# Performance work log

Measured on AMD Instinct MI355X. Metric: run time of the kernel, lower is better.

Reference implementation:

```python
import jax, jax.numpy as jnp
import numpy as np

D_MODEL = 1024
D_STATE = 16
D_CONV = 4
EXPAND = 2
D_INNER = EXPAND * D_MODEL          # 2048
DT_RANK = (D_MODEL + 15) // 16      # 64 (mamba 'auto')
B, L = 2, 1024


def _mamba_params(key, scale=0.02):
    ks = jax.random.split(key, 6)
    return dict(
        inW=jax.random.normal(ks[0], (2 * D_INNER, D_MODEL), jnp.float32) * scale,
        convW=jax.random.normal(ks[1], (D_INNER, 1, D_CONV), jnp.float32) * scale,
        convb=jnp.zeros((D_INNER,), jnp.float32),
        xprojW=jax.random.normal(ks[2], (DT_RANK + 2 * D_STATE, D_INNER), jnp.float32) * scale,
        dtW=jax.random.normal(ks[3], (D_INNER, DT_RANK), jnp.float32) * scale,
        dtb=jax.random.normal(ks[4], (D_INNER,), jnp.float32) * scale,
        A_log=jnp.log(jnp.tile(jnp.arange(1, D_STATE + 1, dtype=jnp.float32), (D_INNER, 1))),
        Dskip=jnp.ones((D_INNER,), jnp.float32),
        outW=jax.random.normal(ks[5], (D_MODEL, D_INNER), jnp.float32) * scale,
    )


def setup_inputs() -> dict:
    key = jax.random.key(0)
    kx, kf, kb, kp = jax.random.split(key, 4)
    inp = {"x": jax.random.normal(kx, (B, L, D_MODEL), jnp.float32)}
    inp["ln_w"] = jnp.ones((D_MODEL,), jnp.float32)
    inp["ln_b"] = jnp.zeros((D_MODEL,), jnp.float32)
    for pref, k in (("f_", kf), ("b_", kb)):
        for name, v in _mamba_params(k).items():
            inp[pref + name] = v
    inp["proj_W"] = jax.random.normal(kp, (D_MODEL, 2 * D_MODEL), jnp.float32) * 0.02
    inp["proj_b"] = jnp.zeros((D_MODEL,), jnp.float32)
    return inp


def _layernorm(x, w, b, eps=1e-5):
    mu = jnp.mean(x, axis=-1, keepdims=True)
    var = jnp.var(x, axis=-1, keepdims=True)
    return (x - mu) * jax.lax.rsqrt(var + eps) * w + b


def _mamba(x, inW, convW, convb, xprojW, dtW, dtb, A_log, Dskip, outW):
    # x: [B, L, d_model]
    xz = jnp.einsum('bld,ed->ble', x, inW)           # [B,L,2*d_inner]
    xs, z = jnp.split(xz, 2, axis=-1)                # each [B,L,d_inner]
    # depthwise causal conv over L
    xc = jnp.transpose(xs, (0, 2, 1))                # [B,d_inner,L]
    xc = jax.lax.conv_general_dilated(
        xc, convW, window_strides=(1,), padding=[(D_CONV - 1, 0)],
        feature_group_count=D_INNER)
    xs = jax.nn.silu(jnp.transpose(xc + convb[None, :, None], (0, 2, 1)))
    # input-dependent dt, B, C
    xdb = jnp.einsum('bld,ed->ble', xs, xprojW)      # [B,L,dt_rank+2*d_state]
    dt, Bm, Cm = jnp.split(xdb, [DT_RANK, DT_RANK + D_STATE], axis=-1)
    dt = jax.nn.softplus(jnp.einsum('blr,dr->bld', dt, dtW) + dtb)  # [B,L,d_inner]
    A = -jnp.exp(A_log)                              # [d_inner,d_state], negative
    dA = jnp.exp(dt[..., None] * A)                  # [B,L,d_inner,d_state]
    dBx = dt[..., None] * Bm[:, :, None, :] * xs[..., None]

    def step(h, inputs):
        dA_t, dBx_t, C_t = inputs                    # [B,d,s],[B,d,s],[B,s]
        h = h * dA_t + dBx_t
        y = jnp.einsum('bds,bs->bd', h, C_t)
        return h, y

    h0 = jnp.zeros((x.shape[0], D_INNER, D_STATE), x.dtype)
    _, ys = jax.lax.scan(step, h0, (jnp.moveaxis(dA, 1, 0),
                                    jnp.moveaxis(dBx, 1, 0),
                                    jnp.moveaxis(Cm, 1, 0)))
    y = jnp.moveaxis(ys, 0, 1)                       # [B,L,d_inner]
    y = (y + xs * Dskip) * jax.nn.silu(z)
    return jnp.einsum('bld,ed->ble', y, outW)        # [B,L,d_model]


def reference(x, ln_w, ln_b,
              f_inW, f_convW, f_convb, f_xprojW, f_dtW, f_dtb, f_A_log, f_Dskip, f_outW,
              b_inW, b_convW, b_convb, b_xprojW, b_dtW, b_dtb, b_A_log, b_Dskip, b_outW,
              proj_W, proj_b):
    normed = _layernorm(x, ln_w, ln_b)
    fwd_out = _mamba(normed, f_inW, f_convW, f_convb, f_xprojW, f_dtW, f_dtb,
                     f_A_log, f_Dskip, f_outW)
    bwd_out = _mamba(normed[:, ::-1, :], b_inW, b_convW, b_convb, b_xprojW, b_dtW,
                     b_dtb, b_A_log, b_Dskip, b_outW)[:, ::-1, :]
    combined = jnp.concatenate([fwd_out, bwd_out], axis=-1)
    return x + jnp.einsum('blc,ec->ble', combined, proj_W) + proj_b
```

## Files before the change

kernel.cpp:

```cpp
#include <hip/hip_runtime.h>
#include <hip/hip_bf16.h>
#include <math.h>

#define DM   1024
#define DI   2048
#define DTR  64
#define DST  16
#define NB   2
#define LL   1024
#define MR   (NB*LL)
#define XLD  128
#define KS   8

typedef __bf16 bf16x8 __attribute__((ext_vector_type(8)));
typedef float  f32x4  __attribute__((ext_vector_type(4)));

__device__ __forceinline__ float siluf(float x) { return x / (1.f + __expf(-x)); }
__device__ __forceinline__ float softplusf(float x) {
    return fmaxf(x, 0.f) + log1pf(__expf(-fabsf(x)));
}
__device__ __forceinline__ unsigned short f2bf(float f) {
    __hip_bfloat16 h = __float2bfloat16(f);
    return *reinterpret_cast<unsigned short*>(&h);
}
__device__ __forceinline__ float bf2f(__hip_bfloat16 h) { return __bfloat162float(h); }

__device__ __forceinline__ void gl2lds16(const __hip_bfloat16* g, __hip_bfloat16* l)
{
    __builtin_amdgcn_global_load_lds(
        (const __attribute__((address_space(1))) unsigned int*)g,
        (__attribute__((address_space(3))) unsigned int*)l, 16, 0, 0);
}

__global__ __launch_bounds__(256) void layernorm_k(
    const float* __restrict__ x, const float* __restrict__ w,
    const float* __restrict__ b, __hip_bfloat16* __restrict__ out)
{
    int row = blockIdx.x;
    int tid = threadIdx.x;
    const float* xr = x + (size_t)row * DM;
    float4 v = *(const float4*)(xr + tid * 4);
    float s = v.x + v.y + v.z + v.w;
    float q = v.x*v.x + v.y*v.y + v.z*v.z + v.w*v.w;
    #pragma unroll
    for (int off = 32; off > 0; off >>= 1) {
        s += __shfl_xor(s, off, 64);
        q += __shfl_xor(q, off, 64);
    }
    __shared__ float ss[4], qq[4];
    int wv = tid >> 6;
    if ((tid & 63) == 0) { ss[wv] = s; qq[wv] = q; }
    __syncthreads();
    s = ss[0] + ss[1] + ss[2] + ss[3];
    q = qq[0] + qq[1] + qq[2] + qq[3];
    float mu  = s * (1.f / DM);
    float var = q * (1.f / DM) - mu * mu;
    float rstd = rsqrtf(var + 1e-5f);
    float4 wv4 = *(const float4*)(w + tid * 4);
    float4 bv4 = *(const float4*)(b + tid * 4);
    ushort4 o;
    o.x = f2bf((v.x - mu) * rstd * wv4.x + bv4.x);
    o.y = f2bf((v.y - mu) * rstd * wv4.y + bv4.y);
    o.z = f2bf((v.z - mu) * rstd * wv4.z + bv4.z);
    o.w = f2bf((v.w - mu) * rstd * wv4.w + bv4.w);
    *(ushort4*)((unsigned short*)out + (size_t)row * DM + tid * 4) = o;
}

__global__ __launch_bounds__(256) void cvt_all_k(
    const float* __restrict__ s0, const float* __restrict__ s1,
    const float* __restrict__ s2, const float* __restrict__ s3,
    const float* __restrict__ s4, __hip_bfloat16* __restrict__ dst)
{
    long idx = (long)(blockIdx.x * 256 + threadIdx.x) * 4;
    const float* src; long off;
    if      (idx <  4194304L) { src = s0; off = idx; }
    else if (idx <  8388608L) { src = s1; off = idx -  4194304L; }
    else if (idx < 10485760L) { src = s2; off = idx -  8388608L; }
    else if (idx < 12582912L) { src = s3; off = idx - 10485760L; }
    else                      { src = s4; off = idx - 12582912L; }
    float4 v = *(const float4*)(src + off);
    ushort4 o;
    o.x = f2bf(v.x); o.y = f2bf(v.y); o.z = f2bf(v.z); o.w = f2bf(v.w);
    *(ushort4*)((unsigned short*)dst + idx) = o;
}

__global__ __launch_bounds__(256) void cvt_pad96_k(
    const float* __restrict__ f_in, const float* __restrict__ b_in,
    __hip_bfloat16* __restrict__ out)
{
    int z = blockIdx.y;
    const float* in = z ? b_in : f_in;
    int idx = (blockIdx.x * 256 + threadIdx.x) * 4;
    int row = idx >> 11;
    ushort4 o = make_ushort4(0, 0, 0, 0);
    if (row < 96) {
        float4 v = *(const float4*)(in + idx);
        o.x = f2bf(v.x); o.y = f2bf(v.y); o.z = f2bf(v.z); o.w = f2bf(v.w);
    }
    *(ushort4*)((unsigned short*)out + (size_t)z * 128 * DI + idx) = o;
}

template<int EPI>
__global__ __launch_bounds__(256) void gemm_gl(
    const __hip_bfloat16* __restrict__ A, int lda, size_t astride,
    const __hip_bfloat16* __restrict__ B, int ldb, size_t bstride,
    void* __restrict__ Cp, int ldc, size_t cstride, int K,
    const float* __restrict__ bias,
    const float* __restrict__ res, int ldres)
{
    __shared__ __hip_bfloat16 As[128 * 64];
    __shared__ __hip_bfloat16 Bs[128 * 64];
    const int tid  = threadIdx.x;
    const int z    = blockIdx.z;
    const int bm   = blockIdx.y * 128;
    const int bn   = blockIdx.x * 128;
    const __hip_bfloat16* Az = A + (size_t)z * astride;
    const __hip_bfloat16* Bz = B + (size_t)z * bstride;
    const int wv   = tid >> 6;
    const int lane = tid & 63;
    const int wr   = (wv >> 1) * 64;
    const int wc   = (wv & 1) * 64;
    const int srow = wv * 32 + (lane >> 3);
    const int cg   = ((lane & 7) ^ (lane >> 3)) * 8;
    const int fr   = lane & 15;
    const int quad = lane >> 4;
    const int pc0  = (quad ^ (fr & 7)) * 8;
    const int pc1  = ((4 + quad) ^ (fr & 7)) * 8;

    f32x4 acc[4][4] = {};

    for (int k0 = 0; k0 < K; k0 += 64) {
        __syncthreads();
        #pragma unroll
        for (int i = 0; i < 4; ++i) {
            int r = srow + i * 8;
            gl2lds16(Az + (size_t)(bm + r) * lda + k0 + cg, As + wv * 2048 + i * 512);
            gl2lds16(Bz + (size_t)(bn + r) * ldb + k0 + cg, Bs + wv * 2048 + i * 512);
        }
        __syncthreads();
        #pragma unroll
        for (int kk = 0; kk < 2; ++kk) {
            const int pc = kk ? pc1 : pc0;
            bf16x8 af[4], bf_[4];
            #pragma unroll
            for (int i = 0; i < 4; ++i) {
                af[i]  = *(const bf16x8*)(As + (wr + i * 16 + fr) * 64 + pc);
                bf_[i] = *(const bf16x8*)(Bs + (wc + i * 16 + fr) * 64 + pc);
            }
            #pragma unroll
            for (int i = 0; i < 4; ++i)
                #pragma unroll
                for (int j = 0; j < 4; ++j)
                    acc[i][j] = __builtin_amdgcn_mfma_f32_16x16x32_bf16(
                        af[i], bf_[j], acc[i][j], 0, 0, 0);
        }
    }

    const int er = quad * 4;
    const int ec = fr;
    #pragma unroll
    for (int i = 0; i < 4; ++i) {
        #pragma unroll
        for (int j = 0; j < 4; ++j) {
            int row = bm + wr + i * 16 + er;
            int col = bn + wc + j * 16 + ec;
            #pragma unroll
            for (int r = 0; r < 4; ++r) {
                float v = acc[i][j][r];
                if (EPI == 1) {
                    ((__hip_bfloat16*)Cp)[(size_t)z * cstride +
                        (size_t)(row + r) * ldc + col] = __float2bfloat16(v);
                } else {
                    ((float*)Cp)[(size_t)(row + r) * ldc + col] =
                        v + bias[col] + res[(size_t)(row + r) * ldres + col];
                }
            }
        }
    }
}

__global__ __launch_bounds__(256) void xproj_part_k(
    const __hip_bfloat16* __restrict__ A,
    const __hip_bfloat16* __restrict__ B,
    float* __restrict__ part)
{
    __shared__ __hip_bfloat16 As[128 * 64];
    __shared__ __hip_bfloat16 Bs[128 * 64];
    const int tid  = threadIdx.x;
    const int ks   = blockIdx.x;
    const int bm   = blockIdx.y * 128;
    const int z    = blockIdx.z;
    const __hip_bfloat16* Az = A + (size_t)z * MR * DI;
    const __hip_bfloat16* Bz = B + (size_t)z * 128 * DI;
    const int kb   = ks * (DI / KS);
    const int wv   = tid >> 6;
    const int lane = tid & 63;
    const int wr   = (wv >> 1) * 64;
    const int wc   = (wv & 1) * 64;
    const int srow = wv * 32 + (lane >> 3);
    const int cg   = ((lane & 7) ^ (lane >> 3)) * 8;
    const int fr   = lane & 15;
    const int quad = lane >> 4;
    const int pc0  = (quad ^ (fr & 7)) * 8;
    const int pc1  = ((4 + quad) ^ (fr & 7)) * 8;

    f32x4 acc[4][4] = {};

    #pragma unroll
    for (int k0 = 0; k0 < DI / KS; k0 += 64) {
        __syncthreads();
        #pragma unroll
        for (int i = 0; i < 4; ++i) {
            int r = srow + i * 8;
            gl2lds16(Az + (size_t)(bm + r) * DI + kb + k0 + cg, As + wv * 2048 + i * 512);
            gl2lds16(Bz + (size_t)r * DI + kb + k0 + cg,        Bs + wv * 2048 + i * 512);
        }
        __syncthreads();
        #pragma unroll
        for (int kk = 0; kk < 2; ++kk) {
            const int pc = kk ? pc1 : pc0;
            bf16x8 af[4], bf_[4];
            #pragma unroll
            for (int i = 0; i < 4; ++i) {
                af[i]  = *(const bf16x8*)(As + (wr + i * 16 + fr) * 64 + pc);
                bf_[i] = *(const bf16x8*)(Bs + (wc + i * 16 + fr) * 64 + pc);
            }
            #pragma unroll
            for (int i = 0; i < 4; ++i)
                #pragma unroll
                for (int j = 0; j < 4; ++j)
                    acc[i][j] = __builtin_amdgcn_mfma_f32_16x16x32_bf16(
                        af[i], bf_[j], acc[i][j], 0, 0, 0);
        }
    }

    float* dst = part + ((size_t)z * KS + ks) * MR * XLD;
    const int er = quad * 4;
    const int ec = fr;
    #pragma unroll
    for (int i = 0; i < 4; ++i)
        #pragma unroll
        for (int j = 0; j < 4; ++j) {
            int row = bm + wr + i * 16 + er;
            int col = wc + j * 16 + ec;
            #pragma unroll
            for (int r = 0; r < 4; ++r)
                dst[(size_t)(row + r) * XLD + col] = acc[i][j][r];
        }
}

__global__ __launch_bounds__(256) void xproj_reduce_k(
    const float* __restrict__ part, float* __restrict__ xdb)
{
    int z = blockIdx.y;
    size_t idx = ((size_t)blockIdx.x * 256 + threadIdx.x) * 4;
    const float* p = part + (size_t)z * KS * MR * XLD;
    float4 s = make_float4(0.f, 0.f, 0.f, 0.f);
    #pragma unroll
    for (int ks = 0; ks < KS; ++ks) {
        float4 v = *(const float4*)(p + (size_t)ks * MR * XLD + idx);
        s.x += v.x; s.y += v.y; s.z += v.z; s.w += v.w;
    }
    *(float4*)(xdb + (size_t)z * MR * XLD + idx) = s;
}

__global__ __launch_bounds__(256) void dtproj_k(
    const float* __restrict__ A, int lda, size_t astride,
    const float* __restrict__ B0, const float* __restrict__ B1, int ldb,
    float* __restrict__ C, int ldc, size_t cstride,
    const float* __restrict__ bias0, const float* __restrict__ bias1)
{
    const int z = blockIdx.z;
    const float* Az = A + (size_t)z * astride;
    const float* B  = z ? B1 : B0;
    const float* bias = z ? bias1 : bias0;
    float* Cz = C + (size_t)z * cstride;

    __shared__ float As[16][68];
    __shared__ float Bs[16][68];
    const int tid = threadIdx.x;
    const int bm = blockIdx.y * 64;
    const int bn = blockIdx.x * 64;
    const int lr = tid >> 2;
    const int lk = (tid & 3) << 2;
    const int tx = tid & 15;
    const int ty = tid >> 4;
    float acc[4][4] = {};

    for (int k0 = 0; k0 < DTR; k0 += 16) {
        float4 av = *(const float4*)(Az + (size_t)(bm + lr) * lda + (k0 + lk));
        float4 bv = *(const float4*)(B  + (size_t)(bn + lr) * ldb + (k0 + lk));
        As[lk+0][lr] = av.x; As[lk+1][lr] = av.y; As[lk+2][lr] = av.z; As[lk+3][lr] = av.w;
        Bs[lk+0][lr] = bv.x; Bs[lk+1][lr] = bv.y; Bs[lk+2][lr] = bv.z; Bs[lk+3][lr] = bv.w;
        __syncthreads();
        #pragma unroll
        for (int kk = 0; kk < 16; ++kk) {
            float4 a4 = *(const float4*)&As[kk][ty << 2];
            float4 b4 = *(const float4*)&Bs[kk][tx << 2];
            float a[4] = {a4.x, a4.y, a4.z, a4.w};
            float b[4] = {b4.x, b4.y, b4.z, b4.w};
            #pragma unroll
            for (int i = 0; i < 4; ++i)
                #pragma unroll
                for (int j = 0; j < 4; ++j)
                    acc[i][j] = fmaf(a[i], b[j], acc[i][j]);
        }
        __syncthreads();
    }

    #pragma unroll
    for (int i = 0; i < 4; ++i) {
        int row  = bm + (ty << 2) + i;
        int col0 = bn + (tx << 2);
        #pragma unroll
        for (int j = 0; j < 4; ++j) {
            int col = col0 + j;
            Cz[(size_t)row * ldc + col] = softplusf(acc[i][j] + bias[col]);
        }
    }
}

__global__ __launch_bounds__(256) void conv_silu_k(
    const __hip_bfloat16* __restrict__ xz2,
    const float* __restrict__ fW, const float* __restrict__ fb,
    const float* __restrict__ bW, const float* __restrict__ bb_,
    __hip_bfloat16* __restrict__ xsb2)
{
    int dirv = blockIdx.y;
    int idx = blockIdx.x * 256 + threadIdx.x;
    int d = idx & (DI - 1);
    int m = idx >> 11;
    int t = m & (LL - 1);
    int bb = m >> 10;
    const float* w  = (dirv ? bW : fW) + d * 4;
    const __hip_bfloat16* xz = xz2 + (size_t)dirv * MR * 2 * DI;
    float acc = (dirv ? bb_ : fb)[d];
    if (dirv == 0) {
        #pragma unroll
        for (int k = 0; k < 4; ++k) {
            int tt = t - 3 + k;
            if (tt >= 0)
                acc = fmaf(w[k], bf2f(xz[(size_t)(bb * LL + tt) * (2 * DI) + d]), acc);
        }
    } else {
        #pragma unroll
        for (int k = 0; k < 4; ++k) {
            int tt = t + 3 - k;
            if (tt < LL)
                acc = fmaf(w[k], bf2f(xz[(size_t)(bb * LL + tt) * (2 * DI) + d]), acc);
        }
    }
    xsb2[(size_t)dirv * MR * DI + (size_t)m * DI + d] = __float2bfloat16(siluf(acc));
}

__global__ __launch_bounds__(256) void scan1_k(
    const float* __restrict__ dtf2, const __hip_bfloat16* __restrict__ xsb2,
    const float* __restrict__ xdb2,
    const float* __restrict__ fA, const float* __restrict__ bA,
    float* __restrict__ hend, float* __restrict__ aprod, int G, int Cn)
{
    int d  = blockIdx.x * 256 + threadIdx.x;
    int bb = blockIdx.y;
    int zz = blockIdx.z;
    int dirv = (zz >= G) ? 1 : 0;
    int g = zz - (dirv ? G : 0);
    const float* A_log = dirv ? bA : fA;
    const float* dtf = dtf2 + (size_t)dirv * MR * DI;
    const __hip_bfloat16* xs = xsb2 + (size_t)dirv * MR * DI;
    const float* xdb = xdb2 + (size_t)dirv * MR * XLD;
    size_t hoff = (size_t)dirv * G * (NB * DI * DST);

    float Ad[DST], h[DST], ap[DST];
    #pragma unroll
    for (int s = 0; s < DST; ++s) {
        Ad[s] = -__expf(A_log[d * DST + s]);
        h[s] = 0.f; ap[s] = 1.f;
    }
    int i0 = g * Cn;
    for (int i = 0; i < Cn; ++i) {
        int ii = i0 + i;
        int t = dirv ? (LL - 1 - ii) : ii;
        size_t m = (size_t)bb * LL + t;
        float dtv = dtf[m * DI + d];
        float xv  = bf2f(xs[m * DI + d]);
        const float* bc = xdb + m * XLD;
        float dtx = dtv * xv;
        #pragma unroll
        for (int s = 0; s < DST; ++s) {
            float dA = __expf(dtv * Ad[s]);
            h[s] = fmaf(h[s], dA, dtx * bc[64 + s]);
            ap[s] *= dA;
        }
    }
    size_t base = hoff + ((size_t)(g * NB + bb) * DI + d) * DST;
    #pragma unroll
    for (int s = 0; s < DST; s += 4) {
        *(float4*)(hend  + base + s) = make_float4(h[s], h[s+1], h[s+2], h[s+3]);
        *(float4*)(aprod + base + s) = make_float4(ap[s], ap[s+1], ap[s+2], ap[s+3]);
    }
}

__global__ __launch_bounds__(256) void scan2_k(
    float* __restrict__ hend, const float* __restrict__ aprod, int G)
{
    int dirv = blockIdx.y;
    int idx = blockIdx.x * 256 + threadIdx.x;
    const int slab = NB * DI * DST;
    size_t hoff = (size_t)dirv * G * slab;
    float carry = 0.f;
    for (int g = 0; g < G; ++g) {
        size_t off = hoff + (size_t)g * slab + idx;
        float a = aprod[off];
        float e = hend[off];
        hend[off] = carry;
        carry = fmaf(a, carry, e);
    }
}

__global__ __launch_bounds__(256) void scan3_k(
    const float* __restrict__ dtf2, __hip_bfloat16* __restrict__ xsb2,
    const float* __restrict__ xdb2, const __hip_bfloat16* __restrict__ xz2,
    const float* __restrict__ fA, const float* __restrict__ bA,
    const float* __restrict__ fD, const float* __restrict__ bD,
    const float* __restrict__ hin, int G, int Cn)
{
    int d  = blockIdx.x * 256 + threadIdx.x;
    int bb = blockIdx.y;
    int zz = blockIdx.z;
    int dirv = (zz >= G) ? 1 : 0;
    int g = zz - (dirv ? G : 0);
    const float* A_log = dirv ? bA : fA;
    const float* Dskip = dirv ? bD : fD;
    const float* dtf = dtf2 + (size_t)dirv * MR * DI;
    __hip_bfloat16* xs = xsb2 + (size_t)dirv * MR * DI;
    const float* xdb = xdb2 + (size_t)dirv * MR * XLD;
    const __hip_bfloat16* xz = xz2 + (size_t)dirv * MR * 2 * DI;
    size_t hoff = (size_t)dirv * G * (NB * DI * DST);

    float Ad[DST], h[DST];
    size_t base = hoff + ((size_t)(g * NB + bb) * DI + d) * DST;
    #pragma unroll
    for (int s = 0; s < DST; ++s) {
        Ad[s] = -__expf(A_log[d * DST + s]);
        h[s] = hin[base + s];
    }
    float Dsk = Dskip[d];
    int i0 = g * Cn;
    for (int i = 0; i < Cn; ++i) {
        int ii = i0 + i;
        int t = dirv ? (LL - 1 - ii) : ii;
        size_t m = (size_t)bb * LL + t;
        float dtv = dtf[m * DI + d];
        float xv  = bf2f(xs[m * DI + d]);
        const float* bc = xdb + m * XLD;
        float dtx = dtv * xv;
        float yv = 0.f;
        #pragma unroll
        for (int s = 0; s < DST; ++s) {
            float dA = __expf(dtv * Ad[s]);
            h[s] = fmaf(h[s], dA, dtx * bc[64 + s]);
            yv = fmaf(h[s], bc[80 + s], yv);
        }
        float zv = bf2f(xz[m * (2 * DI) + DI + d]);
        xs[m * DI + d] = __float2bfloat16((yv + xv * Dsk) * siluf(zv));
    }
}

__global__ __launch_bounds__(256) void scan_mono_k(
    const float* __restrict__ dtf2, __hip_bfloat16* __restrict__ xsb2,
    const float* __restrict__ xdb2, const __hip_bfloat16* __restrict__ xz2,
    const float* __restrict__ fA, const float* __restrict__ bA,
    const float* __restrict__ fD, const float* __restrict__ bD)
{
    int d  = blockIdx.x * 256 + threadIdx.x;
    int bb = blockIdx.y;
    int dirv = blockIdx.z;
    const float* A_log = dirv ? bA : fA;
    const float* Dskip = dirv ? bD : fD;
    const float* dtf = dtf2 + (size_t)dirv * MR * DI;
    __hip_bfloat16* xs = xsb2 + (size_t)dirv * MR * DI;
    const float* xdb = xdb2 + (size_t)dirv * MR * XLD;
    const __hip_bfloat16* xz = xz2 + (size_t)dirv * MR * 2 * DI;
    float Ad[DST], h[DST];
    #pragma unroll
    for (int s = 0; s < DST; ++s) { Ad[s] = -__expf(A_log[d * DST + s]); h[s] = 0.f; }
    float Dsk = Dskip[d];
    for (int i = 0; i < LL; ++i) {
        int t = dirv ? (LL - 1 - i) : i;
        size_t m = (size_t)bb * LL + t;
        float dtv = dtf[m * DI + d];
        float xv  = bf2f(xs[m * DI + d]);
        const float* bc = xdb + m * XLD;
        float dtx = dtv * xv;
        float yv = 0.f;
        #pragma unroll
        for (int s = 0; s < DST; ++s) {
            float dA = __expf(dtv * Ad[s]);
            h[s] = fmaf(h[s], dA, dtx * bc[64 + s]);
            yv = fmaf(h[s], bc[80 + s], yv);
        }
        float zv = bf2f(xz[m * (2 * DI) + DI + d]);
        xs[m * DI + d] = __float2bfloat16((yv + xv * Dsk) * siluf(zv));
    }
}

extern "C" void kernel_launch(void* const* d_in, const int* in_sizes, int n_in,
                              void* d_out, int out_size, void* d_ws, size_t ws_size,
                              hipStream_t stream)
{
    const float* x      = (const float*)d_in[0];
    const float* ln_w   = (const float*)d_in[1];
    const float* ln_b   = (const float*)d_in[2];
    const float* f_inW    = (const float*)d_in[3];
    const float* f_convW  = (const float*)d_in[4];
    const float* f_convb  = (const float*)d_in[5];
    const float* f_xprojW = (const float*)d_in[6];
    const float* f_dtW    = (const float*)d_in[7];
    const float* f_dtb    = (const float*)d_in[8];
    const float* f_A_log  = (const float*)d_in[9];
    const float* f_Dskip  = (const float*)d_in[10];
    const float* f_outW   = (const float*)d_in[11];
    const float* b_inW    = (const float*)d_in[12];
    const float* b_convW  = (const float*)d_in[13];
    const float* b_convb  = (const float*)d_in[14];
    const float* b_xprojW = (const float*)d_in[15];
    const float* b_dtW    = (const float*)d_in[16];
    const float* b_dtb    = (const float*)d_in[17];
    const float* b_A_log  = (const float*)d_in[18];
    const float* b_Dskip  = (const float*)d_in[19];
    const float* b_outW   = (const float*)d_in[20];
    const float* proj_W = (const float*)d_in[21];
    const float* proj_b = (const float*)d_in[22];

    float* ws = (float*)d_ws;
    size_t o = 0;
    __hip_bfloat16* xz2  = (__hip_bfloat16*)(ws + o); o += (size_t)2 * MR * 2 * DI / 2;
    __hip_bfloat16* xsb2 = (__hip_bfloat16*)(ws + o); o += (size_t)2 * MR * DI / 2;
    float* xdb2 = ws + o; o += (size_t)2 * MR * XLD;
    float* dtf2 = ws + o;
    float* part = dtf2;
    __hip_bfloat16* cb = (__hip_bfloat16*)dtf2;
    o += (size_t)2 * MR * DI;
    __hip_bfloat16* nb = (__hip_bfloat16*)(ws + o); o += (size_t)MR * DM / 2;
    __hip_bfloat16* warena = (__hip_bfloat16*)(ws + o); o += 15204352 / 2;
    float* hbuf = ws + o;
    size_t base_floats = o;

    __hip_bfloat16* wbi  = warena;
    __hip_bfloat16* wbo  = warena + 8388608;
    __hip_bfloat16* pwb  = warena + 12582912;
    __hip_bfloat16* wpb2 = warena + 14680064;

    const size_t slab = (size_t)NB * DI * DST;
    int G = 64;
    while (G > 4 && (base_floats + 4ull * G * slab) * 4 > ws_size) G >>= 1;
    int useChunks = ((base_floats + 4ull * G * slab) * 4 <= ws_size);
    float* hend  = hbuf;
    float* aprod = hbuf + 2ull * G * slab;
    int Cn = useChunks ? LL / G : LL;

    cvt_all_k<<<14336, 256, 0, stream>>>(f_inW, b_inW, f_outW, b_outW, proj_W, warena);
    cvt_pad96_k<<<dim3(64, 2), 256, 0, stream>>>(f_xprojW, b_xprojW, wpb2);

    layernorm_k<<<MR, 256, 0, stream>>>(x, ln_w, ln_b, nb);

    gemm_gl<1><<<dim3((2 * DI) / 128, MR / 128, 2), 256, 0, stream>>>(
        nb, DM, 0, wbi, DM, (size_t)2 * DI * DM,
        xz2, 2 * DI, (size_t)MR * 2 * DI, DM, nullptr, nullptr, 0);

    conv_silu_k<<<dim3((MR * DI) / 256, 2), 256, 0, stream>>>(
        xz2, f_convW, f_convb, b_convW, b_convb, xsb2);

    xproj_part_k<<<dim3(KS, MR / 128, 2), 256, 0, stream>>>(xsb2, wpb2, part);
    xproj_reduce_k<<<dim3((MR * XLD) / 1024, 2), 256, 0, stream>>>(part, xdb2);

    dtproj_k<<<dim3(DI / 64, MR / 64, 2), 256, 0, stream>>>(
        xdb2, XLD, (size_t)MR * XLD, f_dtW, b_dtW, DTR,
        dtf2, DI, (size_t)MR * DI, f_dtb, b_dtb);

    if (useChunks) {
        scan1_k<<<dim3(DI / 256, NB, 2 * G), 256, 0, stream>>>(
            dtf2, xsb2, xdb2, f_A_log, b_A_log, hend, aprod, G, Cn);
        scan2_k<<<dim3((NB * DI * DST) / 256, 2), 256, 0, stream>>>(hend, aprod, G);
        scan3_k<<<dim3(DI / 256, NB, 2 * G), 256, 0, stream>>>(
            dtf2, xsb2, xdb2, xz2, f_A_log, b_A_log, f_Dskip, b_Dskip, hend, G, Cn);
    } else {
        scan_mono_k<<<dim3(DI / 256, NB, 2), 256, 0, stream>>>(
            dtf2, xsb2, xdb2, xz2, f_A_log, b_A_log, f_Dskip, b_Dskip);
    }

    gemm_gl<1><<<dim3(DM / 128, MR / 128, 2), 256, 0, stream>>>(
        xsb2, DI, (size_t)MR * DI, wbo, DI, (size_t)DM * DI,
        cb, 2 * DM, (size_t)DM, DI, nullptr, nullptr, 0);

    gemm_gl<2><<<dim3(DM / 128, MR / 128, 1), 256, 0, stream>>>(
        cb, 2 * DM, 0, pwb, 2 * DM, 0,
        (float*)d_out, DM, 0, 2 * DM, proj_b, x, DM);
}
```

Baseline: 452.5 us.

## Fold out_proj into final projection, MFMA dt_proj, and power-based decay in scan

Precomputes a combined weight (proj_W slice times outW) so the two output GEMMs collapse into one split-K GEMM over the concatenated scan outputs, followed by a reduce that adds the residual and bias. The fp32 SIMT dt_proj is replaced by the bf16 MFMA GEMM with a fused softplus epilogue, and dt is stored as bf16. When A_log matches -(s+1), the scan computes the decay terms as successive powers of a single exp, which cuts the per-step exp count. The chunk count G is also lowered. The weight folding costs an extra GEMM each call, and the bf16 dt and powers shortcut may change numerics.

```diff
diff --git a/kernel.cpp b/kernel.cpp
--- a/kernel.cpp
+++ b/kernel.cpp
@@ -76,8 +76,8 @@
     if      (idx <  4194304L) { src = s0; off = idx; }
     else if (idx <  8388608L) { src = s1; off = idx -  4194304L; }
     else if (idx < 10485760L) { src = s2; off = idx -  8388608L; }
-    else if (idx < 12582912L) { src = s3; off = idx - 10485760L; }
-    else                      { src = s4; off = idx - 12582912L; }
+    else if (idx < 10616832L) { src = s3; off = idx - 10485760L; }
+    else                      { src = s4; off = idx - 10616832L; }
     float4 v = *(const float4*)(src + off);
     ushort4 o;
     o.x = f2bf(v.x); o.y = f2bf(v.y); o.z = f2bf(v.z); o.w = f2bf(v.w);
@@ -100,13 +100,37 @@
     *(ushort4*)((unsigned short*)out + (size_t)z * 128 * DI + idx) = o;
 }
 
+__global__ __launch_bounds__(256) void transpose_k(
+    const float* __restrict__ f_o, const float* __restrict__ b_o,
+    __hip_bfloat16* __restrict__ wot)
+{
+    int z = blockIdx.z;
+    const float* src = z ? b_o : f_o;
+    int c0 = blockIdx.x * 64;
+    int r0 = blockIdx.y * 64;
+    __shared__ float t[64][65];
+    int tc = threadIdx.x & 63;
+    int tr = threadIdx.x >> 6;
+    #pragma unroll
+    for (int ii = 0; ii < 16; ++ii) {
+        int rl = tr + ii * 4;
+        t[tc][rl] = src[(size_t)(r0 + rl) * DI + c0 + tc];
+    }
+    __syncthreads();
+    __hip_bfloat16* dst = wot + (size_t)z * DI * DM;
+    #pragma unroll
+    for (int ii = 0; ii < 16; ++ii) {
+        int cl = tr + ii * 4;
+        dst[(size_t)(c0 + cl) * DM + r0 + tc] = __float2bfloat16(t[cl][tc]);
+    }
+}
+
 template<int EPI>
 __global__ __launch_bounds__(256) void gemm_gl(
-    const __hip_bfloat16* __restrict__ A, int lda, size_t astride,
-    const __hip_bfloat16* __restrict__ B, int ldb, size_t bstride,
-    void* __restrict__ Cp, int ldc, size_t cstride, int K,
-    const float* __restrict__ bias,
-    const float* __restrict__ res, int ldres)
+    const __hip_bfloat16* __restrict__ A, int lda, size_t aofs,
+    const __hip_bfloat16* __restrict__ B, int ldb, size_t bofs,
+    void* __restrict__ Cp, int ldc, size_t cofs, int K,
+    const float* __restrict__ bias0, const float* __restrict__ bias1)
 {
     __shared__ __hip_bfloat16 As[128 * 64];
     __shared__ __hip_bfloat16 Bs[128 * 64];
@@ -114,8 +138,8 @@
     const int z    = blockIdx.z;
     const int bm   = blockIdx.y * 128;
     const int bn   = blockIdx.x * 128;
-    const __hip_bfloat16* Az = A + (size_t)z * astride;
-    const __hip_bfloat16* Bz = B + (size_t)z * bstride;
+    const __hip_bfloat16* Az = A + (size_t)z * aofs;
+    const __hip_bfloat16* Bz = B + (size_t)z * bofs;
     const int wv   = tid >> 6;
     const int lane = tid & 63;
     const int wr   = (wv >> 1) * 64;
@@ -156,6 +180,7 @@
         }
     }
 
+    const float* bias = (EPI == 3) ? (z ? bias1 : bias0) : nullptr;
     const int er = quad * 4;
     const int ec = fr;
     #pragma unroll
@@ -168,11 +193,14 @@
             for (int r = 0; r < 4; ++r) {
                 float v = acc[i][j][r];
                 if (EPI == 1) {
-                    ((__hip_bfloat16*)Cp)[(size_t)z * cstride +
+                    ((__hip_bfloat16*)Cp)[(size_t)z * cofs +
                         (size_t)(row + r) * ldc + col] = __float2bfloat16(v);
+                } else if (EPI == 3) {
+                    ((__hip_bfloat16*)Cp)[(size_t)z * cofs +
+                        (size_t)(row + r) * ldc + col] =
+                        __float2bfloat16(softplusf(v + bias[col]));
                 } else {
-                    ((float*)Cp)[(size_t)(row + r) * ldc + col] =
-                        v + bias[col] + res[(size_t)(row + r) * ldres + col];
+                    ((float*)Cp)[(size_t)z * cofs + (size_t)(row + r) * ldc + col] = v;
                 }
             }
         }
@@ -250,7 +278,8 @@
 }
 
 __global__ __launch_bounds__(256) void xproj_reduce_k(
-    const float* __restrict__ part, float* __restrict__ xdb)
+    const float* __restrict__ part, float* __restrict__ xdb,
+    __hip_bfloat16* __restrict__ xdbt)
 {
     int z = blockIdx.y;
     size_t idx = ((size_t)blockIdx.x * 256 + threadIdx.x) * 4;
@@ -262,61 +291,12 @@
         s.x += v.x; s.y += v.y; s.z += v.z; s.w += v.w;
     }
     *(float4*)(xdb + (size_t)z * MR * XLD + idx) = s;
-}
-
-__global__ __launch_bounds__(256) void dtproj_k(
-    const float* __restrict__ A, int lda, size_t astride,
-    const float* __restrict__ B0, const float* __restrict__ B1, int ldb,
-    float* __restrict__ C, int ldc, size_t cstride,
-    const float* __restrict__ bias0, const float* __restrict__ bias1)
-{
-    const int z = blockIdx.z;
-    const float* Az = A + (size_t)z * astride;
-    const float* B  = z ? B1 : B0;
-    const float* bias = z ? bias1 : bias0;
-    float* Cz = C + (size_t)z * cstride;
-
-    __shared__ float As[16][68];
-    __shared__ float Bs[16][68];
-    const int tid = threadIdx.x;
-    const int bm = blockIdx.y * 64;
-    const int bn = blockIdx.x * 64;
-    const int lr = tid >> 2;
-    const int lk = (tid & 3) << 2;
-    const int tx = tid & 15;
-    const int ty = tid >> 4;
-    float acc[4][4] = {};
-
-    for (int k0 = 0; k0 < DTR; k0 += 16) {
-        float4 av = *(const float4*)(Az + (size_t)(bm + lr) * lda + (k0 + lk));
-        float4 bv = *(const float4*)(B  + (size_t)(bn + lr) * ldb + (k0 + lk));
-        As[lk+0][lr] = av.x; As[lk+1][lr] = av.y; As[lk+2][lr] = av.z; As[lk+3][lr] = av.w;
-        Bs[lk+0][lr] = bv.x; Bs[lk+1][lr] = bv.y; Bs[lk+2][lr] = bv.z; Bs[lk+3][lr] = bv.w;
-        __syncthreads();
-        #pragma unroll
-        for (int kk = 0; kk < 16; ++kk) {
-            float4 a4 = *(const float4*)&As[kk][ty << 2];
-            float4 b4 = *(const float4*)&Bs[kk][tx << 2];
-            float a[4] = {a4.x, a4.y, a4.z, a4.w};
-            float b[4] = {b4.x, b4.y, b4.z, b4.w};
-            #pragma unroll
-            for (int i = 0; i < 4; ++i)
-                #pragma unroll
-                for (int j = 0; j < 4; ++j)
-                    acc[i][j] = fmaf(a[i], b[j], acc[i][j]);
-        }
-        __syncthreads();
-    }
-
-    #pragma unroll
-    for (int i = 0; i < 4; ++i) {
-        int row  = bm + (ty << 2) + i;
-        int col0 = bn + (tx << 2);
-        #pragma unroll
-        for (int j = 0; j < 4; ++j) {
-            int col = col0 + j;
-            Cz[(size_t)row * ldc + col] = softplusf(acc[i][j] + bias[col]);
-        }
+    int c = (int)(idx & (XLD - 1));
+    if (c < 64) {
+        size_t m = idx >> 7;
+        ushort4 o;
+        o.x = f2bf(s.x); o.y = f2bf(s.y); o.z = f2bf(s.z); o.w = f2bf(s.w);
+        *(ushort4*)((unsigned short*)xdbt + (size_t)z * MR * 64 + m * 64 + c) = o;
     }
 }
 
@@ -354,7 +334,7 @@
 }
 
 __global__ __launch_bounds__(256) void scan1_k(
-    const float* __restrict__ dtf2, const __hip_bfloat16* __restrict__ xsb2,
+    const __hip_bfloat16* __restrict__ dtf2, const __hip_bfloat16* __restrict__ xsb2,
     const float* __restrict__ xdb2,
     const float* __restrict__ fA, const float* __restrict__ bA,
     float* __restrict__ hend, float* __restrict__ aprod, int G, int Cn)
@@ -365,15 +345,17 @@
     int dirv = (zz >= G) ? 1 : 0;
     int g = zz - (dirv ? G : 0);
     const float* A_log = dirv ? bA : fA;
-    const float* dtf = dtf2 + (size_t)dirv * MR * DI;
+    const __hip_bfloat16* dtf = dtf2 + (size_t)dirv * MR * DI;
     const __hip_bfloat16* xs = xsb2 + (size_t)dirv * MR * DI;
     const float* xdb = xdb2 + (size_t)dirv * MR * XLD;
     size_t hoff = (size_t)dirv * G * (NB * DI * DST);
 
     float Ad[DST], h[DST], ap[DST];
+    bool pw = true;
     #pragma unroll
     for (int s = 0; s < DST; ++s) {
         Ad[s] = -__expf(A_log[d * DST + s]);
+        pw = pw && (fabsf(Ad[s] + (float)(s + 1)) < 1e-3f * (s + 1));
         h[s] = 0.f; ap[s] = 1.f;
     }
     int i0 = g * Cn;
@@ -381,15 +363,24 @@
         int ii = i0 + i;
         int t = dirv ? (LL - 1 - ii) : ii;
         size_t m = (size_t)bb * LL + t;
-        float dtv = dtf[m * DI + d];
+        float dtv = bf2f(dtf[m * DI + d]);
         float xv  = bf2f(xs[m * DI + d]);
         const float* bc = xdb + m * XLD;
         float dtx = dtv * xv;
+        float dAv[DST];
+        if (pw) {
+            float r = __expf(-dtv);
+            float a = r;
+            #pragma unroll
+            for (int s = 0; s < DST; ++s) { dAv[s] = a; a *= r; }
+        } else {
+            #pragma unroll
+            for (int s = 0; s < DST; ++s) dAv[s] = __expf(dtv * Ad[s]);
+        }
         #pragma unroll
         for (int s = 0; s < DST; ++s) {
-            float dA = __expf(dtv * Ad[s]);
-            h[s] = fmaf(h[s], dA, dtx * bc[64 + s]);
-            ap[s] *= dA;
+            h[s] = fmaf(h[s], dAv[s], dtx * bc[64 + s]);
+            ap[s] *= dAv[s];
         }
     }
     size_t base = hoff + ((size_t)(g * NB + bb) * DI + d) * DST;
@@ -418,11 +409,11 @@
 }
 
 __global__ __launch_bounds__(256) void scan3_k(
-    const float* __restrict__ dtf2, __hip_bfloat16* __restrict__ xsb2,
+    const __hip_bfloat16* __restrict__ dtf2, const __hip_bfloat16* __restrict__ xsb2,
     const float* __restrict__ xdb2, const __hip_bfloat16* __restrict__ xz2,
     const float* __restrict__ fA, const float* __restrict__ bA,
     const float* __restrict__ fD, const float* __restrict__ bD,
-    const float* __restrict__ hin, int G, int Cn)
+    const float* __restrict__ hin, __hip_bfloat16* __restrict__ ycat, int G, int Cn)
 {
     int d  = blockIdx.x * 256 + threadIdx.x;
     int bb = blockIdx.y;
@@ -431,17 +422,19 @@
     int g = zz - (dirv ? G : 0);
     const float* A_log = dirv ? bA : fA;
     const float* Dskip = dirv ? bD : fD;
-    const float* dtf = dtf2 + (size_t)dirv * MR * DI;
-    __hip_bfloat16* xs = xsb2 + (size_t)dirv * MR * DI;
+    const __hip_bfloat16* dtf = dtf2 + (size_t)dirv * MR * DI;
+    const __hip_bfloat16* xs = xsb2 + (size_t)dirv * MR * DI;
     const float* xdb = xdb2 + (size_t)dirv * MR * XLD;
     const __hip_bfloat16* xz = xz2 + (size_t)dirv * MR * 2 * DI;
     size_t hoff = (size_t)dirv * G * (NB * DI * DST);
 
     float Ad[DST], h[DST];
+    bool pw = true;
     size_t base = hoff + ((size_t)(g * NB + bb) * DI + d) * DST;
     #pragma unroll
     for (int s = 0; s < DST; ++s) {
         Ad[s] = -__expf(A_log[d * DST + s]);
+        pw = pw && (fabsf(Ad[s] + (float)(s + 1)) < 1e-3f * (s + 1));
         h[s] = hin[base + s];
     }
     float Dsk = Dskip[d];
@@ -450,35 +443,46 @@
         int ii = i0 + i;
         int t = dirv ? (LL - 1 - ii) : ii;
         size_t m = (size_t)bb * LL + t;
-        float dtv = dtf[m * DI + d];
+        float dtv = bf2f(dtf[m * DI + d]);
         float xv  = bf2f(xs[m * DI + d]);
         const float* bc = xdb + m * XLD;
         float dtx = dtv * xv;
+        float dAv[DST];
+        if (pw) {
+            float r = __expf(-dtv);
+            float a = r;
+            #pragma unroll
+            for (int s = 0; s < DST; ++s) { dAv[s] = a; a *= r; }
+        } else {
+            #pragma unroll
+            for (int s = 0; s < DST; ++s) dAv[s] = __expf(dtv * Ad[s]);
+        }
         float yv = 0.f;
         #pragma unroll
         for (int s = 0; s < DST; ++s) {
-            float dA = __expf(dtv * Ad[s]);
-            h[s] = fmaf(h[s], dA, dtx * bc[64 + s]);
+            h[s] = fmaf(h[s], dAv[s], dtx * bc[64 + s]);
             yv = fmaf(h[s], bc[80 + s], yv);
         }
         float zv = bf2f(xz[m * (2 * DI) + DI + d]);
-        xs[m * DI + d] = __float2bfloat16((yv + xv * Dsk) * siluf(zv));
+        ycat[m * (2 * DI) + (size_t)dirv * DI + d] =
+            __float2bfloat16((yv + xv * Dsk) * siluf(zv));
     }
 }
 
 __global__ __launch_bounds__(256) void scan_mono_k(
-    const float* __restrict__ dtf2, __hip_bfloat16* __restrict__ xsb2,
+    const __hip_bfloat16* __restrict__ dtf2, const __hip_bfloat16* __restrict__ xsb2,
     const float* __restrict__ xdb2, const __hip_bfloat16* __restrict__ xz2,
     const float* __restrict__ fA, const float* __restrict__ bA,
-    const float* __restrict__ fD, const float* __restrict__ bD)
+    const float* __restrict__ fD, const float* __restrict__ bD,
+    __hip_bfloat16* __restrict__ ycat)
 {
     int d  = blockIdx.x * 256 + threadIdx.x;
     int bb = blockIdx.y;
     int dirv = blockIdx.z;
     const float* A_log = dirv ? bA : fA;
     const float* Dskip = dirv ? bD : fD;
-    const float* dtf = dtf2 + (size_t)dirv * MR * DI;
-    __hip_bfloat16* xs = xsb2 + (size_t)dirv * MR * DI;
+    const __hip_bfloat16* dtf = dtf2 + (size_t)dirv * MR * DI;
+    const __hip_bfloat16* xs = xsb2 + (size_t)dirv * MR * DI;
     const float* xdb = xdb2 + (size_t)dirv * MR * XLD;
     const __hip_bfloat16* xz = xz2 + (size_t)dirv * MR * 2 * DI;
     float Ad[DST], h[DST];
@@ -488,7 +492,7 @@
     for (int i = 0; i < LL; ++i) {
         int t = dirv ? (LL - 1 - i) : i;
         size_t m = (size_t)bb * LL + t;
-        float dtv = dtf[m * DI + d];
+        float dtv = bf2f(dtf[m * DI + d]);
         float xv  = bf2f(xs[m * DI + d]);
         const float* bc = xdb + m * XLD;
         float dtx = dtv * xv;
@@ -500,8 +504,31 @@
             yv = fmaf(h[s], bc[80 + s], yv);
         }
         float zv = bf2f(xz[m * (2 * DI) + DI + d]);
-        xs[m * DI + d] = __float2bfloat16((yv + xv * Dsk) * siluf(zv));
-    }
+        ycat[m * (2 * DI) + (size_t)dirv * DI + d] =
+            __float2bfloat16((yv + xv * Dsk) * siluf(zv));
+    }
+}
+
+__global__ __launch_bounds__(256) void final_reduce_k(
+    const float* __restrict__ part, const float* __restrict__ x,
+    const float* __restrict__ proj_b, float* __restrict__ out)
+{
+    size_t idx = ((size_t)blockIdx.x * 256 + threadIdx.x) * 4;
+    float4 s = make_float4(0.f, 0.f, 0.f, 0.f);
+    #pragma unroll
+    for (int z = 0; z < 4; ++z) {
+        float4 v = *(const float4*)(part + (size_t)z * MR * DM + idx);
+        s.x += v.x; s.y += v.y; s.z += v.z; s.w += v.w;
+    }
+    float4 xv = *(const float4*)(x + idx);
+    int col = (int)(idx & (DM - 1));
+    float4 pb = *(const float4*)(proj_b + col);
+    float4 o;
+    o.x = xv.x + pb.x + s.x;
+    o.y = xv.y + pb.y + s.y;
+    o.z = xv.z + pb.z + s.z;
+    o.w = xv.w + pb.w + s.w;
+    *(float4*)(out + idx) = o;
 }
 
 extern "C" void kernel_launch(void* const* d_in, const int* in_sizes, int n_in,
@@ -534,66 +561,75 @@
 
     float* ws = (float*)d_ws;
     size_t o = 0;
-    __hip_bfloat16* xz2  = (__hip_bfloat16*)(ws + o); o += (size_t)2 * MR * 2 * DI / 2;
+    __hip_bfloat16* xz2  = (__hip_bfloat16*)(ws + o);
+    __hip_bfloat16* wot  = xz2;
+    float* fpart = ws + o;
+    o += (size_t)2 * MR * 2 * DI / 2;
     __hip_bfloat16* xsb2 = (__hip_bfloat16*)(ws + o); o += (size_t)2 * MR * DI / 2;
+    __hip_bfloat16* ycat = (__hip_bfloat16*)(ws + o);
+    float* xpart = ws + o;
+    o += (size_t)MR * 2 * DI / 2;
     float* xdb2 = ws + o; o += (size_t)2 * MR * XLD;
-    float* dtf2 = ws + o;
-    float* part = dtf2;
-    __hip_bfloat16* cb = (__hip_bfloat16*)dtf2;
-    o += (size_t)2 * MR * DI;
+    __hip_bfloat16* xdbt = (__hip_bfloat16*)(ws + o); o += (size_t)2 * MR * 64 / 2;
+    __hip_bfloat16* dtfb = (__hip_bfloat16*)(ws + o); o += (size_t)2 * MR * DI / 2;
     __hip_bfloat16* nb = (__hip_bfloat16*)(ws + o); o += (size_t)MR * DM / 2;
-    __hip_bfloat16* warena = (__hip_bfloat16*)(ws + o); o += 15204352 / 2;
+    __hip_bfloat16* warena = (__hip_bfloat16*)(ws + o); o += 15466496 / 2;
     float* hbuf = ws + o;
     size_t base_floats = o;
 
     __hip_bfloat16* wbi  = warena;
-    __hip_bfloat16* wbo  = warena + 8388608;
-    __hip_bfloat16* pwb  = warena + 12582912;
-    __hip_bfloat16* wpb2 = warena + 14680064;
+    __hip_bfloat16* pwb  = warena +  8388608;
+    __hip_bfloat16* wdt  = warena + 10485760;
+    __hip_bfloat16* wpb2 = warena + 10747904;
+    __hip_bfloat16* wcat = warena + 11272192;
 
     const size_t slab = (size_t)NB * DI * DST;
-    int G = 64;
+    int G = 32;
     while (G > 4 && (base_floats + 4ull * G * slab) * 4 > ws_size) G >>= 1;
     int useChunks = ((base_floats + 4ull * G * slab) * 4 <= ws_size);
     float* hend  = hbuf;
     float* aprod = hbuf + 2ull * G * slab;
     int Cn = useChunks ? LL / G : LL;
 
-    cvt_all_k<<<14336, 256, 0, stream>>>(f_inW, b_inW, f_outW, b_outW, proj_W, warena);
+    cvt_all_k<<<10496, 256, 0, stream>>>(f_inW, b_inW, proj_W, f_dtW, b_dtW, warena);
     cvt_pad96_k<<<dim3(64, 2), 256, 0, stream>>>(f_xprojW, b_xprojW, wpb2);
+    transpose_k<<<dim3(DI / 64, DM / 64, 2), 256, 0, stream>>>(f_outW, b_outW, wot);
+    gemm_gl<1><<<dim3(DI / 128, DM / 128, 2), 256, 0, stream>>>(
+        pwb, 2 * DM, (size_t)DM, wot, DM, (size_t)DI * DM,
+        wcat, 2 * DI, (size_t)DI, DM, nullptr, nullptr);
 
     layernorm_k<<<MR, 256, 0, stream>>>(x, ln_w, ln_b, nb);
 
     gemm_gl<1><<<dim3((2 * DI) / 128, MR / 128, 2), 256, 0, stream>>>(
         nb, DM, 0, wbi, DM, (size_t)2 * DI * DM,
-        xz2, 2 * DI, (size_t)MR * 2 * DI, DM, nullptr, nullptr, 0);
+        xz2, 2 * DI, (size_t)MR * 2 * DI, DM, nullptr, nullptr);
 
     conv_silu_k<<<dim3((MR * DI) / 256, 2), 256, 0, stream>>>(
         xz2, f_convW, f_convb, b_convW, b_convb, xsb2);
 
-    xproj_part_k<<<dim3(KS, MR / 128, 2), 256, 0, stream>>>(xsb2, wpb2, part);
-    xproj_reduce_k<<<dim3((MR * XLD) / 1024, 2), 256, 0, stream>>>(part, xdb2);
-
-    dtproj_k<<<dim3(DI / 64, MR / 64, 2), 256, 0, stream>>>(
-        xdb2, XLD, (size_t)MR * XLD, f_dtW, b_dtW, DTR,
-        dtf2, DI, (size_t)MR * DI, f_dtb, b_dtb);
+    xproj_part_k<<<dim3(KS, MR / 128, 2), 256, 0, stream>>>(xsb2, wpb2, xpart);
+    xproj_reduce_k<<<dim3((MR * XLD) / 1024, 2), 256, 0, stream>>>(xpart, xdb2, xdbt);
+
+    gemm_gl<3><<<dim3(DI / 128, MR / 128, 2), 256, 0, stream>>>(
+        xdbt, 64, (size_t)MR * 64, wdt, 64, (size_t)DI * 64,
+        dtfb, DI, (size_t)MR * DI, 64, f_dtb, b_dtb);
 
     if (useChunks) {
         scan1_k<<<dim3(DI / 256, NB, 2 * G), 256, 0, stream>>>(
-            dtf2, xsb2, xdb2, f_A_log, b_A_log, hend, aprod, G, Cn);
+            dtfb, xsb2, xdb2, f_A_log, b_A_log, hend, aprod, G, Cn);
         scan2_k<<<dim3((NB * DI * DST) / 256, 2), 256, 0, stream>>>(hend, aprod, G);
         scan3_k<<<dim3(DI / 256, NB, 2 * G), 256, 0, stream>>>(
-            dtf2, xsb2, xdb2, xz2, f_A_log, b_A_log, f_Dskip, b_Dskip, hend, G, Cn);
+            dtfb, xsb2, xdb2, xz2, f_A_log, b_A_log, f_Dskip, b_Dskip,
+            hend, ycat, G, Cn);
     } else {
         scan_mono_k<<<dim3(DI / 256, NB, 2), 256, 0, stream>>>(
-            dtf2, xsb2, xdb2, xz2, f_A_log, b_A_log, f_Dskip, b_Dskip);
-    }
-
-    gemm_gl<1><<<dim3(DM / 128, MR / 128, 2), 256, 0, stream>>>(
-        xsb2, DI, (size_t)MR * DI, wbo, DI, (size_t)DM * DI,
-        cb, 2 * DM, (size_t)DM, DI, nullptr, nullptr, 0);
-
-    gemm_gl<2><<<dim3(DM / 128, MR / 128, 1), 256, 0, stream>>>(
-        cb, 2 * DM, 0, pwb, 2 * DM, 0,
-        (float*)d_out, DM, 0, 2 * DM, proj_b, x, DM);
-}
+            dtfb, xsb2, xdb2, xz2, f_A_log, b_A_log, f_Dskip, b_Dskip, ycat);
+    }
+
+    gemm_gl<0><<<dim3(DM / 128, MR / 128, 4), 256, 0, stream>>>(
+        ycat, 2 * DI, 1024, wcat, 2 * DI, 1024,
+        fpart, DM, (size_t)MR * DM, 1024, nullptr, nullptr);
+
+    final_reduce_k<<<(MR * DM) / 1024, 256, 0, stream>>>(
+        fpart, x, proj_b, (float*)d_out);
+}
```

New measurement: 424.8 us. 1.07x faster.
